# Kernel optimization log

Hardware: AMD Instinct MI355X
Metric: run time of the kernel (lower is better)

Reference implementation:

```python
import jax, jax.numpy as jnp
import numpy as np

NUM_HEADS = 12
EMBED_DIM = 768
HEAD_DIM = EMBED_DIM // NUM_HEADS


def setup_inputs() -> dict:
    key = jax.random.key(0)
    ks = jax.random.split(key, 9)
    B, S, D = 8, 1025, EMBED_DIM
    s = 1.0 / np.sqrt(D)
    return {
        "x": jax.random.normal(ks[0], (B, S, D), dtype=jnp.float32),
        "Wk": jax.random.normal(ks[1], (D, D), dtype=jnp.float32) * s,
        "bk": jnp.zeros((D,), dtype=jnp.float32),
        "Wq": jax.random.normal(ks[2], (D, D), dtype=jnp.float32) * s,
        "bq": jnp.zeros((D,), dtype=jnp.float32),
        "Wv": jax.random.normal(ks[3], (D, D), dtype=jnp.float32) * s,
        "bv": jnp.zeros((D,), dtype=jnp.float32),
        "Wp": jax.random.normal(ks[4], (D, D), dtype=jnp.float32) * s,
        "bp": jnp.zeros((D,), dtype=jnp.float32),
    }


def reference(x, Wk, bk, Wq, bq, Wv, bv, Wp, bp):
    B, S, D = x.shape
    H, Hd = NUM_HEADS, HEAD_DIM
    # Linear projections (torch Linear: y = x @ W^T + b)
    k = (x @ Wk.T + bk).reshape(B, S, H, Hd).transpose(0, 2, 1, 3)  # (B,H,S,Hd)
    q = (x @ Wq.T + bq).reshape(B, S, H, Hd).transpose(0, 2, 1, 3)
    v = (x @ Wv.T + bv).reshape(B, S, H, Hd).transpose(0, 2, 1, 3)
    scale = 1.0 / jnp.sqrt(jnp.asarray(Hd, dtype=x.dtype))
    scores = jnp.einsum("bhqd,bhkd->bhqk", q, k) * scale  # (B,H,S,S)
    attn = jax.nn.softmax(scores, axis=-1)
    # dropout is identity at inference (eval mode)
    out = jnp.einsum("bhqk,bhkd->bhqd", attn, v)  # (B,H,S,Hd)
    out = out.transpose(0, 2, 1, 3).reshape(B, S, D)
    return out @ Wp.T + bp
```

## Files before the change

kernel.cpp:

```cpp
#include <hip/hip_runtime.h>
#include <stdint.h>

#define BATCH  8
#define SEQ    1025
#define DMODEL 768
#define NHEAD  12
#define HDIM   64
#define MTOT   (BATCH * SEQ)
#define MPAD   8320
#define SPAD   1056
#define BHTOT  (BATCH * NHEAD)
#define QT32   33
#define NTILE  17
#define NKSTEP 12
#define QKSCALE 0.18033688011112042f

typedef __bf16 bf16x8 __attribute__((ext_vector_type(8)));
typedef __bf16 bf16x4 __attribute__((ext_vector_type(4)));
typedef float  f32x4  __attribute__((ext_vector_type(4)));
typedef float  f32x16 __attribute__((ext_vector_type(16)));

#if __has_builtin(__builtin_amdgcn_exp2f)
#define EXP2F __builtin_amdgcn_exp2f
#else
#define EXP2F exp2f
#endif

constexpr size_t XB_OFF  = 0;
constexpr size_t XB_SZ   = (size_t)MPAD * DMODEL * 2;
constexpr size_t W_SZ    = (size_t)DMODEL * DMODEL * 2;
constexpr size_t WQB_OFF = XB_OFF + XB_SZ;
constexpr size_t WKB_OFF = WQB_OFF + W_SZ;
constexpr size_t WVB_OFF = WKB_OFF + W_SZ;
constexpr size_t WPB_OFF = WVB_OFF + W_SZ;
constexpr size_t QB_OFF  = WPB_OFF + W_SZ;
constexpr size_t QB_SZ   = (size_t)BHTOT * SEQ * HDIM * 2;
constexpr size_t KB_OFF  = QB_OFF + QB_SZ;
constexpr size_t VT_OFF  = KB_OFF + QB_SZ;
constexpr size_t VT_SZ   = (size_t)BHTOT * HDIM * SPAD * 2;
constexpr size_t AO_OFF  = XB_OFF;
constexpr size_t WS_NEEDED = VT_OFF + VT_SZ;

__device__ __forceinline__ void async16(const void* g, void* l) {
  __builtin_amdgcn_global_load_lds((__attribute__((address_space(1))) void*)g,
                                   (__attribute__((address_space(3))) void*)l,
                                   16, 0, 0);
}

__device__ __forceinline__ unsigned pkbf(float lo, float hi) {
  __bf16 l = (__bf16)lo, h = (__bf16)hi;
  unsigned short lb = __builtin_bit_cast(unsigned short, l);
  unsigned short hb = __builtin_bit_cast(unsigned short, h);
  return ((unsigned)hb << 16) | (unsigned)lb;
}
__device__ __forceinline__ unsigned shfl32u(unsigned x) {
  return (unsigned)__shfl_xor((int)x, 32, 64);
}
__device__ __forceinline__ float pairmax(float x) {
  return fmaxf(x, __shfl_xor(x, 32, 64));
}
__device__ __forceinline__ float pairsum(float x) {
  return x + __shfl_xor(x, 32, 64);
}

__device__ __forceinline__ float tree_max16(const f32x16& s) {
  float a0 = fmaxf(s[0], s[1]),   a1 = fmaxf(s[2], s[3]);
  float a2 = fmaxf(s[4], s[5]),   a3 = fmaxf(s[6], s[7]);
  float a4 = fmaxf(s[8], s[9]),   a5 = fmaxf(s[10], s[11]);
  float a6 = fmaxf(s[12], s[13]), a7 = fmaxf(s[14], s[15]);
  float b0 = fmaxf(a0, a1), b1 = fmaxf(a2, a3);
  float b2 = fmaxf(a4, a5), b3 = fmaxf(a6, a7);
  return fmaxf(fmaxf(b0, b1), fmaxf(b2, b3));
}
__device__ __forceinline__ float tree_sum16(const f32x16& s) {
  float a0 = s[0] + s[1],   a1 = s[2] + s[3];
  float a2 = s[4] + s[5],   a3 = s[6] + s[7];
  float a4 = s[8] + s[9],   a5 = s[10] + s[11];
  float a6 = s[12] + s[13], a7 = s[14] + s[15];
  float b0 = a0 + a1, b1 = a2 + a3, b2 = a4 + a5, b3 = a6 + a7;
  return (b0 + b1) + (b2 + b3);
}

__global__ void __launch_bounds__(256)
convert_f32_bf16(const float* __restrict__ src, __bf16* __restrict__ dst,
                 int n_src, int n_dst) {
  int idx = (blockIdx.x * 256 + threadIdx.x) * 4;
  if (idx >= n_dst) return;
  bf16x4 o;
  if (idx + 3 < n_src) {
    float4 v = *(const float4*)&src[idx];
    o[0] = (__bf16)v.x; o[1] = (__bf16)v.y; o[2] = (__bf16)v.z; o[3] = (__bf16)v.w;
  } else {
    #pragma unroll
    for (int t = 0; t < 4; ++t) {
      int k = idx + t;
      o[t] = (k < n_src) ? (__bf16)src[k] : (__bf16)0.f;
    }
  }
  *(bf16x4*)&dst[idx] = o;
}

__global__ void __launch_bounds__(256)
convert_w4(const float* __restrict__ w0, const float* __restrict__ w1,
           const float* __restrict__ w2, const float* __restrict__ w3,
           __bf16* __restrict__ dst) {
  const int which = blockIdx.y;
  const float* src = (which == 0) ? w0 : (which == 1) ? w1 : (which == 2) ? w2 : w3;
  __bf16* d = dst + (size_t)which * DMODEL * DMODEL;
  int idx = (blockIdx.x * 256 + threadIdx.x) * 4;
  if (idx >= DMODEL * DMODEL) return;
  float4 v = *(const float4*)&src[idx];
  bf16x4 o;
  o[0] = (__bf16)v.x; o[1] = (__bf16)v.y; o[2] = (__bf16)v.z; o[3] = (__bf16)v.w;
  *(bf16x4*)&d[idx] = o;
}

__device__ __forceinline__ void stage_tile(const __bf16* __restrict__ A,
                                           const __bf16* __restrict__ W,
                                           __bf16* As, __bf16* Bs,
                                           int m0, int n0, int kt, int tid) {
  #pragma unroll
  for (int i = 0; i < 4; ++i) {
    const int gi = i * 256 + tid;
    const int r  = gi >> 3;
    const int p  = gi & 7;
    const int g  = p ^ (r & 7);
    async16(A + (size_t)(m0 + r) * DMODEL + kt + g * 8, As + gi * 8);
    async16(W + (size_t)(n0 + r) * DMODEL + kt + g * 8, Bs + gi * 8);
  }
}

__device__ __forceinline__ void compute_tile(const __bf16* __restrict__ As,
                                             const __bf16* __restrict__ Bs,
                                             f32x4 acc[4][4],
                                             int wm, int wn, int l15, int lg, int rx) {
  #pragma unroll
  for (int kk = 0; kk < 2; ++kk) {
    bf16x8 af[4], bfr[4];
    #pragma unroll
    for (int i = 0; i < 4; ++i)
      af[i] = *(const bf16x8*)&As[(wm * 64 + i * 16 + l15) * 64 + (((kk * 4 + lg) ^ rx)) * 8];
    #pragma unroll
    for (int j = 0; j < 4; ++j)
      bfr[j] = *(const bf16x8*)&Bs[(wn * 64 + j * 16 + l15) * 64 + (((kk * 4 + lg) ^ rx)) * 8];
    #pragma unroll
    for (int i = 0; i < 4; ++i)
      #pragma unroll
      for (int j = 0; j < 4; ++j)
        acc[i][j] = __builtin_amdgcn_mfma_f32_16x16x32_bf16(af[i], bfr[j], acc[i][j], 0, 0, 0);
  }
}

__device__ __forceinline__ void gemm_core(const __bf16* __restrict__ A,
                                          const __bf16* __restrict__ W,
                                          __bf16 (*As)[128 * 64], __bf16 (*Bs)[128 * 64],
                                          int m0, int n0, f32x4 acc[4][4]) {
  const int tid  = threadIdx.x;
  const int lane = tid & 63;
  const int wave = tid >> 6;
  const int wm = wave >> 1, wn = wave & 1;
  const int l15 = lane & 15, lg = lane >> 4;
  const int rx  = l15 & 7;

  stage_tile(A, W, As[0], Bs[0], m0, n0, 0, tid);
  __syncthreads();

  for (int t = 0; t < NKSTEP; ++t) {
    const int cur = t & 1;
    if (t + 1 < NKSTEP)
      stage_tile(A, W, As[cur ^ 1], Bs[cur ^ 1], m0, n0, (t + 1) * 64, tid);
    compute_tile(As[cur], Bs[cur], acc, wm, wn, l15, lg, rx);
    __syncthreads();
  }
}

__global__ void __launch_bounds__(256)
gemm_qkv_kernel(const __bf16* __restrict__ xb, const __bf16* __restrict__ wsb,
                const float* __restrict__ bq, const float* __restrict__ bk,
                const float* __restrict__ bv,
                __bf16* __restrict__ qb, __bf16* __restrict__ kb,
                __bf16* __restrict__ vtb) {
  __shared__ __bf16 As[2][128 * 64];
  __shared__ __bf16 Bs[2][128 * 64];
  const int wg  = blockIdx.x;
  const int xcd = wg & 7, idx = wg >> 3;
  const int v   = xcd * 146 + (xcd < 2 ? xcd : 2) + idx;
  const int m0  = (v / 18) * 128;
  const int n0  = (v % 18) * 128;

  f32x4 acc[4][4];
  #pragma unroll
  for (int i = 0; i < 4; ++i)
    #pragma unroll
    for (int j = 0; j < 4; ++j) acc[i][j] = (f32x4){0.f, 0.f, 0.f, 0.f};

  gemm_core(xb, wsb, As, Bs, m0, n0, acc);

  const int lane = threadIdx.x & 63;
  const int wave = threadIdx.x >> 6;
  const int wm = wave >> 1, wn = wave & 1;
  const int l15 = lane & 15, lg = lane >> 4;
  #pragma unroll
  for (int i = 0; i < 4; ++i) {
    #pragma unroll
    for (int j = 0; j < 4; ++j) {
      const int ncolg = n0 + wn * 64 + j * 16 + l15;
      const int mode = ncolg / 768;
      const int col  = ncolg - mode * 768;
      const float bb = (mode == 0 ? bq : (mode == 1 ? bk : bv))[col];
      const int h = col >> 6, hd = col & 63;
      #pragma unroll
      for (int r = 0; r < 4; ++r) {
        const int mrow = m0 + wm * 64 + i * 16 + lg * 4 + r;
        if (mrow < MTOT) {
          float val = acc[i][j][r] + bb;
          const int b = mrow / SEQ;
          const int s = mrow - b * SEQ;
          const int bh = b * NHEAD + h;
          if (mode == 2)
            vtb[((size_t)bh * HDIM + hd) * SPAD + s] = (__bf16)val;
          else if (mode == 0)
            qb[((size_t)bh * SEQ + s) * HDIM + hd] = (__bf16)(val * QKSCALE);
          else
            kb[((size_t)bh * SEQ + s) * HDIM + hd] = (__bf16)val;
        }
      }
    }
  }
}

__global__ void __launch_bounds__(256)
gemm_proj_kernel(const __bf16* __restrict__ ab, const __bf16* __restrict__ wpb,
                 const float* __restrict__ bp, float* __restrict__ out) {
  __shared__ __bf16 As[2][128 * 64];
  __shared__ __bf16 Bs[2][128 * 64];
  const int wg  = blockIdx.x;
  const int xcd = wg & 7, idx = wg >> 3;
  const int v   = xcd * 48 + (xcd < 6 ? xcd : 6) + idx;
  const int m0  = (v / 6) * 128;
  const int n0  = (v % 6) * 128;

  f32x4 acc[4][4];
  #pragma unroll
  for (int i = 0; i < 4; ++i)
    #pragma unroll
    for (int j = 0; j < 4; ++j) acc[i][j] = (f32x4){0.f, 0.f, 0.f, 0.f};

  gemm_core(ab, wpb, As, Bs, m0, n0, acc);

  const int lane = threadIdx.x & 63;
  const int wave = threadIdx.x >> 6;
  const int wm = wave >> 1, wn = wave & 1;
  const int l15 = lane & 15, lg = lane >> 4;
  #pragma unroll
  for (int i = 0; i < 4; ++i) {
    #pragma unroll
    for (int j = 0; j < 4; ++j) {
      const int ncol = n0 + wn * 64 + j * 16 + l15;
      const float bb = bp[ncol];
      #pragma unroll
      for (int r = 0; r < 4; ++r) {
        const int mrow = m0 + wm * 64 + i * 16 + lg * 4 + r;
        if (mrow < MTOT) out[(size_t)mrow * DMODEL + ncol] = acc[i][j][r] + bb;
      }
    }
  }
}

__device__ __forceinline__ void build_pa(const f32x16& s, int hi, bf16x8 pa[2]) {
  #pragma unroll
  for (int sl2 = 0; sl2 < 2; ++sl2) {
    const int off = sl2 * 8;
    unsigned w0 = pkbf(s[off + 0], s[off + 1]);
    unsigned w1 = pkbf(s[off + 2], s[off + 3]);
    unsigned w2 = pkbf(s[off + 4], s[off + 5]);
    unsigned w3 = pkbf(s[off + 6], s[off + 7]);
    unsigned p0 = shfl32u(w0), p1 = shfl32u(w1);
    unsigned p2 = shfl32u(w2), p3 = shfl32u(w3);
    unsigned pw[4];
    pw[0] = hi ? p2 : w0;
    pw[1] = hi ? p3 : w1;
    pw[2] = hi ? w2 : p0;
    pw[3] = hi ? w3 : p1;
    __builtin_memcpy(&pa[sl2], pw, 16);
  }
}

__device__ __forceinline__ void stage_kv(const __bf16* __restrict__ Kp,
                                         const __bf16* __restrict__ Vp,
                                         __bf16* kls, __bf16* vls,
                                         int k0, int tid) {
  const int r = tid >> 3, p = tid & 7;
  const int g = p ^ (r & 7);
  async16(Kp + (size_t)(k0 + r) * HDIM + g * 8, kls + tid * 8);
  int col = k0 + g * 8;
  if (col >= SPAD) col = 0;
  async16(Vp + (size_t)r * SPAD + col, vls + tid * 8);
}

template<bool MASK>
__device__ __forceinline__ void attn_step(const __bf16* __restrict__ kls,
                                          const __bf16* __restrict__ vls,
                                          int half, const bf16x8 (&qf)[4],
                                          int l31, int hi,
                                          float& mrun, float& lrun,
                                          f32x16& o0, f32x16& o1) {
  const int kr = half * 32 + l31;
  const int krx = kr & 7;

  f32x16 s;
  #pragma unroll
  for (int r = 0; r < 16; ++r) s[r] = 0.f;
  #pragma unroll
  for (int sl = 0; sl < 4; ++sl) {
    bf16x8 kf = *(const bf16x8*)&kls[(kr * 8 + ((2 * sl + hi) ^ krx)) * 8];
    s = __builtin_amdgcn_mfma_f32_32x32x16_bf16(kf, qf[sl], s, 0, 0, 0);
  }
  if (MASK) {
    #pragma unroll
    for (int r = 1; r < 16; ++r) s[r] = -1e30f;
    if (hi) s[0] = -1e30f;
  }

  const float mloc = pairmax(tree_max16(s));
  if (!__all(mloc - mrun <= 8.f)) {
    const float mnew = fmaxf(mrun, mloc);
    const float corr = EXP2F(mrun - mnew);
    lrun *= corr;
    #pragma unroll
    for (int r = 0; r < 16; ++r) { o0[r] *= corr; o1[r] *= corr; }
    mrun = mnew;
  }

  #pragma unroll
  for (int r = 0; r < 16; ++r) s[r] = EXP2F(s[r] - mrun);
  lrun += pairsum(tree_sum16(s));

  bf16x8 pa[2];
  build_pa(s, hi, pa);

  #pragma unroll
  for (int ot = 0; ot < 2; ++ot) {
    const int vr = ot * 32 + l31;
    const int vrx = vr & 7;
    f32x16& o = ot ? o1 : o0;
    #pragma unroll
    for (int j = 0; j < 2; ++j) {
      bf16x8 vf = *(const bf16x8*)&vls[(vr * 8 + ((half * 4 + 2 * j + hi) ^ vrx)) * 8];
      o = __builtin_amdgcn_mfma_f32_32x32x16_bf16(vf, pa[j], o, 0, 0, 0);
    }
  }
}

__global__ void __launch_bounds__(512, 4)
attn_kernel(const __bf16* __restrict__ qb, const __bf16* __restrict__ kb,
            const __bf16* __restrict__ vtb, __bf16* __restrict__ ao) {
  __shared__ __bf16 kls[2][64 * 64];
  __shared__ __bf16 vls[2][64 * 64];

  const int tid  = threadIdx.x;
  const int wid  = tid >> 6;
  const int lane = tid & 63;
  const int l31 = lane & 31, hi = (lane >> 5) & 1;

  const int bid = blockIdx.x;
  const int xcd = bid & 7;
  const int ixd = bid >> 3;
  const int bh  = xcd * (BHTOT / 8) + ixd / 5;
  const int qblk = ixd % 5;
  const int qt  = qblk * 8 + wid;
  const bool active = qt < QT32;

  const __bf16* Qp = qb + (size_t)bh * SEQ * HDIM;
  const __bf16* Kp = kb + (size_t)bh * SEQ * HDIM;
  const __bf16* Vp = vtb + (size_t)bh * HDIM * SPAD;

  const int qidx = qt * 32 + l31;
  const int qc = (qidx < SEQ ? qidx : SEQ - 1);
  bf16x8 qf[4];
  if (active) {
    #pragma unroll
    for (int sl = 0; sl < 4; ++sl)
      qf[sl] = *(const bf16x8*)&Qp[(size_t)qc * HDIM + sl * 16 + hi * 8];
  }

  f32x16 o0, o1;
  #pragma unroll
  for (int r = 0; r < 16; ++r) { o0[r] = 0.f; o1[r] = 0.f; }
  float mrun = -1e30f, lrun = 0.f;

  stage_kv(Kp, Vp, kls[0], vls[0], 0, tid);
  __syncthreads();

  for (int t = 0; t < NTILE; ++t) {
    const int cur = t & 1;
    if (t + 1 < NTILE)
      stage_kv(Kp, Vp, kls[cur ^ 1], vls[cur ^ 1], (t + 1) * 64, tid);
    if (active) {
      if (t < NTILE - 1) {
        attn_step<false>(kls[cur], vls[cur], 0, qf, l31, hi, mrun, lrun, o0, o1);
        attn_step<false>(kls[cur], vls[cur], 1, qf, l31, hi, mrun, lrun, o0, o1);
      } else {
        attn_step<true>(kls[cur], vls[cur], 0, qf, l31, hi, mrun, lrun, o0, o1);
      }
    }
    __syncthreads();
  }

  if (active && qidx < SEQ) {
    const int b = bh / NHEAD, h = bh % NHEAD;
    const float inv = 1.f / lrun;
    __bf16* base = ao + ((size_t)b * SEQ + qidx) * DMODEL + h * HDIM + hi * 4;
    #pragma unroll
    for (int t = 0; t < 2; ++t) {
      const f32x16& o = t ? o1 : o0;
      #pragma unroll
      for (int g = 0; g < 4; ++g) {
        bf16x4 w;
        #pragma unroll
        for (int u = 0; u < 4; ++u) w[u] = (__bf16)(o[g * 4 + u] * inv);
        *(bf16x4*)(base + t * 32 + g * 8) = w;
      }
    }
  }
}

extern "C" void kernel_launch(void* const* d_in, const int* in_sizes, int n_in,
                              void* d_out, int out_size, void* d_ws, size_t ws_size,
                              hipStream_t stream) {
  const float* x  = (const float*)d_in[0];
  const float* Wk = (const float*)d_in[1];
  const float* bk = (const float*)d_in[2];
  const float* Wq = (const float*)d_in[3];
  const float* bq = (const float*)d_in[4];
  const float* Wv = (const float*)d_in[5];
  const float* bv = (const float*)d_in[6];
  const float* Wp = (const float*)d_in[7];
  const float* bp = (const float*)d_in[8];
  float* out = (float*)d_out;

  if (ws_size < WS_NEEDED) return;

  char* ws = (char*)d_ws;
  __bf16* xb  = (__bf16*)(ws + XB_OFF);
  __bf16* wqb = (__bf16*)(ws + WQB_OFF);
  __bf16* wpb = (__bf16*)(ws + WPB_OFF);
  __bf16* qb  = (__bf16*)(ws + QB_OFF);
  __bf16* kb  = (__bf16*)(ws + KB_OFF);
  __bf16* vtb = (__bf16*)(ws + VT_OFF);
  __bf16* ab  = (__bf16*)(ws + AO_OFF);

  hipMemsetAsync(vtb, 0, VT_SZ, stream);

  {
    const int n_src = MTOT * DMODEL, n_dst = MPAD * DMODEL;
    convert_f32_bf16<<<dim3((n_dst / 4 + 255) / 256), dim3(256), 0, stream>>>(x, xb, n_src, n_dst);
    const int nw = DMODEL * DMODEL;
    convert_w4<<<dim3((nw / 4 + 255) / 256, 4), dim3(256), 0, stream>>>(Wq, Wk, Wv, Wp, wqb);
  }

  gemm_qkv_kernel<<<dim3(1170), dim3(256), 0, stream>>>(
      xb, wqb, bq, bk, bv, qb, kb, vtb);

  attn_kernel<<<dim3(8 * (BHTOT / 8) * 5), dim3(512), 0, stream>>>(qb, kb, vtb, ab);

  gemm_proj_kernel<<<dim3(390), dim3(256), 0, stream>>>(ab, wpb, bp, out);
}
```

Baseline: 176.2 us.

## Pipeline GEMM K-loop with partial vmcnt waits, precomputed addresses and MFMA priority

Restructures the projection GEMM main loop so the next K-slice's async global-to-LDS loads are issued before waiting, and the wait uses vmcnt(8) so only the older batch must land. Per-thread global and LDS addresses are computed once outside the loop, and the loop is unrolled by two to use fixed buffer pointers. s_setprio is raised around the MFMA block. This targets load latency exposure and address arithmetic in the loop, at the cost of hand-placed waitcnt and barriers that depend on exact instruction counts.

```diff
diff --git a/kernel.cpp b/kernel.cpp
--- a/kernel.cpp
+++ b/kernel.cpp
@@ -115,41 +115,46 @@
   *(bf16x4*)&d[idx] = o;
 }
 
-__device__ __forceinline__ void stage_tile(const __bf16* __restrict__ A,
-                                           const __bf16* __restrict__ W,
+__device__ __forceinline__ void stage_step(const __bf16* const (&sa)[4],
+                                           const __bf16* const (&sw)[4],
                                            __bf16* As, __bf16* Bs,
-                                           int m0, int n0, int kt, int tid) {
+                                           int kt, int tid) {
   #pragma unroll
   for (int i = 0; i < 4; ++i) {
     const int gi = i * 256 + tid;
-    const int r  = gi >> 3;
-    const int p  = gi & 7;
-    const int g  = p ^ (r & 7);
-    async16(A + (size_t)(m0 + r) * DMODEL + kt + g * 8, As + gi * 8);
-    async16(W + (size_t)(n0 + r) * DMODEL + kt + g * 8, Bs + gi * 8);
-  }
-}
-
-__device__ __forceinline__ void compute_tile(const __bf16* __restrict__ As,
-                                             const __bf16* __restrict__ Bs,
-                                             f32x4 acc[4][4],
-                                             int wm, int wn, int l15, int lg, int rx) {
+    async16(sa[i] + kt, As + gi * 8);
+    async16(sw[i] + kt, Bs + gi * 8);
+  }
+}
+
+__device__ __forceinline__ void compute_tile(const __bf16* __restrict__ pa,
+                                             const __bf16* __restrict__ pb,
+                                             int off0, int off1,
+                                             f32x4 acc[4][4]) {
   #pragma unroll
   for (int kk = 0; kk < 2; ++kk) {
+    const int offk = kk ? off1 : off0;
     bf16x8 af[4], bfr[4];
     #pragma unroll
     for (int i = 0; i < 4; ++i)
-      af[i] = *(const bf16x8*)&As[(wm * 64 + i * 16 + l15) * 64 + (((kk * 4 + lg) ^ rx)) * 8];
+      af[i] = *(const bf16x8*)(pa + i * 1024 + offk);
     #pragma unroll
     for (int j = 0; j < 4; ++j)
-      bfr[j] = *(const bf16x8*)&Bs[(wn * 64 + j * 16 + l15) * 64 + (((kk * 4 + lg) ^ rx)) * 8];
+      bfr[j] = *(const bf16x8*)(pb + j * 1024 + offk);
+    __builtin_amdgcn_s_setprio(1);
     #pragma unroll
     for (int i = 0; i < 4; ++i)
       #pragma unroll
       for (int j = 0; j < 4; ++j)
         acc[i][j] = __builtin_amdgcn_mfma_f32_16x16x32_bf16(af[i], bfr[j], acc[i][j], 0, 0, 0);
-  }
-}
+    __builtin_amdgcn_s_setprio(0);
+  }
+}
+
+#define GC_WAIT8  asm volatile("s_waitcnt vmcnt(8)" ::: "memory")
+#define GC_WAIT0  asm volatile("s_waitcnt vmcnt(0)" ::: "memory")
+#define GC_BAR    __builtin_amdgcn_s_barrier()
+#define GC_SCHED  __builtin_amdgcn_sched_barrier(0)
 
 __device__ __forceinline__ void gemm_core(const __bf16* __restrict__ A,
                                           const __bf16* __restrict__ W,
@@ -162,15 +167,46 @@
   const int l15 = lane & 15, lg = lane >> 4;
   const int rx  = l15 & 7;
 
-  stage_tile(A, W, As[0], Bs[0], m0, n0, 0, tid);
-  __syncthreads();
-
-  for (int t = 0; t < NKSTEP; ++t) {
-    const int cur = t & 1;
-    if (t + 1 < NKSTEP)
-      stage_tile(A, W, As[cur ^ 1], Bs[cur ^ 1], m0, n0, (t + 1) * 64, tid);
-    compute_tile(As[cur], Bs[cur], acc, wm, wn, l15, lg, rx);
-    __syncthreads();
+  const __bf16* sa[4];
+  const __bf16* sw[4];
+  #pragma unroll
+  for (int i = 0; i < 4; ++i) {
+    const int gi = i * 256 + tid;
+    const int r  = gi >> 3;
+    const int g  = (gi & 7) ^ (r & 7);
+    sa[i] = A + (size_t)(m0 + r) * DMODEL + g * 8;
+    sw[i] = W + (size_t)(n0 + r) * DMODEL + g * 8;
+  }
+  const int off0 = ((0 * 4 + lg) ^ rx) * 8;
+  const int off1 = ((1 * 4 + lg) ^ rx) * 8;
+  const __bf16* paA0 = &As[0][(wm * 64 + l15) * 64];
+  const __bf16* paA1 = &As[1][(wm * 64 + l15) * 64];
+  const __bf16* pbB0 = &Bs[0][(wn * 64 + l15) * 64];
+  const __bf16* pbB1 = &Bs[1][(wn * 64 + l15) * 64];
+
+  stage_step(sa, sw, As[0], Bs[0], 0, tid);
+
+  #pragma unroll 1
+  for (int tt = 0; tt < NKSTEP / 2; ++tt) {
+    const int t = tt * 2;
+    stage_step(sa, sw, As[1], Bs[1], (t + 1) * 64, tid);
+    GC_WAIT8;
+    GC_BAR;
+    GC_SCHED;
+    compute_tile(paA0, pbB0, off0, off1, acc);
+    GC_BAR;
+    GC_SCHED;
+    if (t + 2 < NKSTEP) {
+      stage_step(sa, sw, As[0], Bs[0], (t + 2) * 64, tid);
+      GC_WAIT8;
+    } else {
+      GC_WAIT0;
+    }
+    GC_BAR;
+    GC_SCHED;
+    compute_tile(paA1, pbB1, off0, off1, acc);
+    GC_BAR;
+    GC_SCHED;
   }
 }
 
```

After: 171.8 us. 1.03x faster.
